# Performance work log

Measured on AMD Instinct MI355X. Metric: run time of the kernel, lower is better.

## Reference

```python
import jax, jax.numpy as jnp
import numpy as np

D_MODEL = 512
D_QK = 512
H = 8
HEAD_DIM = D_QK // H   # 64
V_DIM = D_MODEL // H   # 64
PROJ_OUT = D_MODEL + 2 * D_QK + H  # 1544


def setup_inputs() -> dict:
    key = jax.random.key(0)
    k1, k2, k3, k4, k5 = jax.random.split(key, 5)
    B, S = 2, 2048
    x = jax.random.normal(k1, (B, S, D_MODEL), dtype=jnp.float32)
    s_in = 1.0 / np.sqrt(D_MODEL)
    Wvqkn_w = jax.random.uniform(k2, (PROJ_OUT, D_MODEL), jnp.float32, -s_in, s_in)
    Wvqkn_b = jax.random.uniform(k3, (PROJ_OUT,), jnp.float32, -s_in, s_in)
    out_w = jax.random.uniform(k4, (D_MODEL, D_MODEL), jnp.float32, -s_in, s_in)
    out_b = jax.random.uniform(k5, (D_MODEL,), jnp.float32, -s_in, s_in)
    return {"x": x, "Wvqkn_w": Wvqkn_w, "Wvqkn_b": Wvqkn_b,
            "out_w": out_w, "out_b": out_b}


def reference(x, Wvqkn_w, Wvqkn_b, out_w, out_b):
    B, S, _ = x.shape
    # fused qkvn projection
    vqkn = jnp.einsum('bsd,od->bso', x, Wvqkn_w) + Wvqkn_b  # [B,S,1544]
    v = vqkn[..., :D_MODEL]                                  # [B,S,512]
    qk = vqkn[..., D_MODEL:D_MODEL + 2 * D_QK]               # [B,S,1024]
    n = vqkn[..., D_MODEL + 2 * D_QK:]                       # [B,S,H]
    qk = qk.reshape(B, S, 2, H, HEAD_DIM)
    v = v.reshape(B, S, H, V_DIM)
    q, k = qk[:, :, 0], qk[:, :, 1]                          # approx_fn = identity
    # linear attention via cumulative KV state (scale=1.0, scale_B=False)
    kv = jnp.einsum('bshd,bsht->bshdt', k, v)                # [B,S,H,D,Dv]
    kv = jnp.cumsum(kv, axis=1)
    out = jnp.einsum('bshd,bshdt->bsht', q, kv)              # [B,S,H,Dv]
    # normalization gating: norm_fn = exp, no offset
    gate = jnp.exp(-jnp.exp(n))                              # [B,S,H]
    ctx = gate[..., None] * out
    ctx = ctx.reshape(B, S, D_MODEL)
    return jnp.einsum('bsd,od->bso', ctx, out_w) + out_b
```

## Files before the change

kernel.cpp:

```cpp
#include <hip/hip_runtime.h>
#include <hip/hip_bf16.h>
#include <math.h>

#define B_    2
#define S_    2048
#define DM    512
#define H_    8
#define PROJ  1544
#define NPAD1 1664
#define CHK   64
#define NC    32
#define BS_   4096
#define BH    16

typedef __attribute__((ext_vector_type(8))) short shortx8;
typedef __attribute__((ext_vector_type(4))) short shortx4;
typedef __attribute__((ext_vector_type(4))) float floatx4;

#define GCAST(p) ((const __attribute__((address_space(1))) void*)(p))
#define LCAST(p) ((__attribute__((address_space(3))) void*)(p))

__device__ inline short f2bf(float f) {
    __hip_bfloat16 h = __float2bfloat16(f);
    return *(short*)&h;
}
__device__ inline float bf2f(short s) {
    __hip_bfloat16 h = *(__hip_bfloat16*)&s;
    return __bfloat162float(h);
}
__device__ inline shortx8 read8(const short* buf, int row, int k) {
    return *(const shortx8*)&buf[row * 64 + ((((k >> 3) ^ (row & 7))) << 3)];
}

#define E1 ((size_t)BS_ * DM)
#define E2 ((size_t)NPAD1 * DM)
#define E3 ((size_t)DM * DM)
__global__ __launch_bounds__(256) void convert_all(const float* __restrict__ x,
                                                   const float* __restrict__ w1,
                                                   const float* __restrict__ w2,
                                                   short* __restrict__ xb,
                                                   short* __restrict__ w1b,
                                                   short* __restrict__ w2b) {
    size_t e = ((size_t)blockIdx.x * 256 + threadIdx.x) * 8;
    const float* src;
    short* dst;
    bool zero = false;
    if (e < E1) { src = x + e; dst = xb + e; }
    else if (e < E1 + E2) {
        size_t o = e - E1;
        dst = w1b + o;
        size_t row = o >> 9;
        if (row < PROJ) src = w1 + o; else { src = w1; zero = true; }
    } else if (e < E1 + E2 + E3) {
        size_t o = e - E1 - E2;
        src = w2 + o; dst = w2b + o;
    } else return;
    short out[8];
    if (zero) {
#pragma unroll
        for (int i = 0; i < 8; i++) out[i] = 0;
    } else {
        float4 f0 = *(const float4*)src;
        float4 f1 = *(const float4*)(src + 4);
        out[0] = f2bf(f0.x); out[1] = f2bf(f0.y); out[2] = f2bf(f0.z); out[3] = f2bf(f0.w);
        out[4] = f2bf(f1.x); out[5] = f2bf(f1.y); out[6] = f2bf(f1.z); out[7] = f2bf(f1.w);
    }
    *(shortx8*)dst = *(shortx8*)out;
}

__global__ __launch_bounds__(256) void gemm_mfma64(const short* __restrict__ A,
                                                   const short* __restrict__ Bw,
                                                   const float* __restrict__ bias,
                                                   float* __restrict__ C,
                                                   int N, int K) {
    __shared__ __align__(16) short As[64 * 64];
    __shared__ __align__(16) short Bs[128 * 64];
    const int tid  = threadIdx.x;
    const int wave = tid >> 6, lane = tid & 63;
    const int m0 = blockIdx.y * 64;
    const int n0 = blockIdx.x * 128;
    const int lrow = lane >> 3;
    const int swz  = ((lane & 7) ^ lrow) << 3;
    const int lm = lane & 15, q = lane >> 4;
    const int wc = wave * 32;
    floatx4 acc[4][2] = {};

    const short* gA0 = A  + (size_t)(m0 +      wave * 8 + lrow) * K + swz;
    const short* gA1 = A  + (size_t)(m0 + 32 + wave * 8 + lrow) * K + swz;
    const short* gB[4];
#pragma unroll
    for (int h = 0; h < 4; h++)
        gB[h] = Bw + (size_t)(n0 + h * 32 + wave * 8 + lrow) * K + swz;

    for (int k0 = 0; k0 < K; k0 += 64) {
        __builtin_amdgcn_global_load_lds(GCAST(gA0 + k0), LCAST(&As[(wave * 8) * 64]),        16, 0, 0);
        __builtin_amdgcn_global_load_lds(GCAST(gA1 + k0), LCAST(&As[(32 + wave * 8) * 64]),   16, 0, 0);
#pragma unroll
        for (int h = 0; h < 4; h++)
            __builtin_amdgcn_global_load_lds(GCAST(gB[h] + k0), LCAST(&Bs[(h * 32 + wave * 8) * 64]), 16, 0, 0);
        __syncthreads();
        shortx8 af[2][4], bw[2][2];
#pragma unroll
        for (int ks = 0; ks < 2; ks++) {
#pragma unroll
            for (int i = 0; i < 4; i++) af[ks][i] = read8(As, i * 16 + lm, ks * 32 + q * 8);
#pragma unroll
            for (int j = 0; j < 2; j++) bw[ks][j] = read8(Bs, wc + j * 16 + lm, ks * 32 + q * 8);
        }
#pragma unroll
        for (int ks = 0; ks < 2; ks++)
#pragma unroll
            for (int i = 0; i < 4; i++)
#pragma unroll
                for (int j = 0; j < 2; j++)
                    acc[i][j] = __builtin_amdgcn_mfma_f32_16x16x32_bf16(af[ks][i], bw[ks][j], acc[i][j], 0, 0, 0);
        __syncthreads();
    }
#pragma unroll
    for (int i = 0; i < 4; i++) {
        int rb = m0 + i * 16 + q * 4;
#pragma unroll
        for (int j = 0; j < 2; j++) {
            int col = n0 + wc + j * 16 + lm;
            float bv = bias[col];
#pragma unroll
            for (int r = 0; r < 4; r++)
                C[(size_t)(rb + r) * N + col] = acc[i][j][r] + bv;
        }
    }
}

__global__ __launch_bounds__(256) void gemm1_fused(const short* __restrict__ A,
                                                   const short* __restrict__ Bw,
                                                   const float* __restrict__ bias,
                                                   short* __restrict__ qb,
                                                   short* __restrict__ kb,
                                                   short* __restrict__ kTb,
                                                   short* __restrict__ vTb,
                                                   float* __restrict__ gateb) {
    __shared__ __align__(16) short As[64 * 64];
    __shared__ __align__(16) short Bs[128 * 64];
    const int K = DM;
    const int tid  = threadIdx.x;
    const int wave = tid >> 6, lane = tid & 63;
    const int m0 = blockIdx.y * 64;
    const int n0 = blockIdx.x * 128;
    const int lrow = lane >> 3;
    const int swz  = ((lane & 7) ^ lrow) << 3;
    const int lm = lane & 15, q = lane >> 4;
    const int wc = wave * 32;
    floatx4 acc[4][2] = {};

    const short* gA0 = A  + (size_t)(m0 +      wave * 8 + lrow) * K + swz;
    const short* gA1 = A  + (size_t)(m0 + 32 + wave * 8 + lrow) * K + swz;
    const short* gB[4];
#pragma unroll
    for (int h = 0; h < 4; h++)
        gB[h] = Bw + (size_t)(n0 + h * 32 + wave * 8 + lrow) * K + swz;

    for (int k0 = 0; k0 < K; k0 += 64) {
        __builtin_amdgcn_global_load_lds(GCAST(gA0 + k0), LCAST(&As[(wave * 8) * 64]),        16, 0, 0);
        __builtin_amdgcn_global_load_lds(GCAST(gA1 + k0), LCAST(&As[(32 + wave * 8) * 64]),   16, 0, 0);
#pragma unroll
        for (int h = 0; h < 4; h++)
            __builtin_amdgcn_global_load_lds(GCAST(gB[h] + k0), LCAST(&Bs[(h * 32 + wave * 8) * 64]), 16, 0, 0);
        __syncthreads();
        shortx8 af[2][4], bw[2][2];
#pragma unroll
        for (int ks = 0; ks < 2; ks++) {
#pragma unroll
            for (int i = 0; i < 4; i++) af[ks][i] = read8(As, i * 16 + lm, ks * 32 + q * 8);
#pragma unroll
            for (int j = 0; j < 2; j++) bw[ks][j] = read8(Bs, wc + j * 16 + lm, ks * 32 + q * 8);
        }
#pragma unroll
        for (int ks = 0; ks < 2; ks++)
#pragma unroll
            for (int i = 0; i < 4; i++)
#pragma unroll
                for (int j = 0; j < 2; j++)
                    acc[i][j] = __builtin_amdgcn_mfma_f32_16x16x32_bf16(af[ks][i], bw[ks][j], acc[i][j], 0, 0, 0);
        __syncthreads();
    }

    const int bIdx = m0 >> 11;
    const int bh0  = bIdx * H_;
#pragma unroll
    for (int i = 0; i < 4; i++) {
        int s0 = (m0 & (S_ - 1)) + i * 16 + q * 4;
#pragma unroll
        for (int j = 0; j < 2; j++) {
            int col = n0 + wc + j * 16 + lm;
            float bv = (col < PROJ) ? bias[col] : 0.f;
            float vals[4];
#pragma unroll
            for (int r = 0; r < 4; r++) vals[r] = acc[i][j][r] + bv;
            if (col < 512) {
                int h = col >> 6, vd = col & 63;
                short tmp[4];
#pragma unroll
                for (int r = 0; r < 4; r++) tmp[r] = f2bf(vals[r]);
                *(shortx4*)&vTb[((size_t)(bh0 + h) * 64 + vd) * S_ + s0] = *(shortx4*)tmp;
            } else if (col < 1024) {
                int h = (col >> 6) - 8, d = col & 63;
                size_t rb = ((size_t)(bh0 + h) * S_ + s0) * 64 + d;
#pragma unroll
                for (int r = 0; r < 4; r++) qb[rb + (size_t)r * 64] = f2bf(vals[r]);
            } else if (col < 1536) {
                int h = (col >> 6) - 16, d = col & 63;
                size_t rb = ((size_t)(bh0 + h) * S_ + s0) * 64 + d;
                short tmp[4];
#pragma unroll
                for (int r = 0; r < 4; r++) { tmp[r] = f2bf(vals[r]); kb[rb + (size_t)r * 64] = tmp[r]; }
                *(shortx4*)&kTb[((size_t)(bh0 + h) * 64 + d) * S_ + s0] = *(shortx4*)tmp;
            } else if (col < PROJ) {
                int h = col - 1536;
                float g[4];
#pragma unroll
                for (int r = 0; r < 4; r++) g[r] = __expf(-__expf(vals[r]));
                *(float4*)&gateb[(size_t)(bh0 + h) * S_ + s0] = make_float4(g[0], g[1], g[2], g[3]);
            }
        }
    }
}

__global__ __launch_bounds__(256) void chunk_kv_mfma(const short* __restrict__ vTb,
                                                     const short* __restrict__ kTb,
                                                     float* __restrict__ kvbuf) {
    __shared__ __align__(16) short VT[64 * 64];
    __shared__ __align__(16) short KT[64 * 64];
    const int blk = blockIdx.x;
    const int c = blk & (NC - 1), bh = blk >> 5;
    const int base = c * CHK;
    const int tid = threadIdx.x, wave = tid >> 6, lane = tid & 63;
    const int lrow = lane >> 3, lgrp = lane & 7;

#pragma unroll
    for (int half = 0; half < 2; half++) {
        int v0 = wave * 8 + half * 32;
        int row = v0 + lrow;
        int gcol = ((lgrp ^ (row & 7)) << 3);
        __builtin_amdgcn_global_load_lds(GCAST(vTb + ((size_t)(bh * 64 + row)) * S_ + base + gcol),
                                         LCAST(&VT[v0 * 64]), 16, 0, 0);
        __builtin_amdgcn_global_load_lds(GCAST(kTb + ((size_t)(bh * 64 + row)) * S_ + base + gcol),
                                         LCAST(&KT[v0 * 64]), 16, 0, 0);
    }
    __syncthreads();

    const int lm = lane & 15, q = lane >> 4;
    const int wr = (wave >> 1) * 32, wc = (wave & 1) * 32;
    floatx4 acc[2][2] = {};
#pragma unroll
    for (int ks = 0; ks < 2; ks++) {
        shortx8 a[2], b2[2];
#pragma unroll
        for (int i = 0; i < 2; i++) a[i]  = read8(VT, wr + i * 16 + lm, ks * 32 + q * 8);
#pragma unroll
        for (int j = 0; j < 2; j++) b2[j] = read8(KT, wc + j * 16 + lm, ks * 32 + q * 8);
#pragma unroll
        for (int i = 0; i < 2; i++)
#pragma unroll
            for (int j = 0; j < 2; j++)
                acc[i][j] = __builtin_amdgcn_mfma_f32_16x16x32_bf16(a[i], b2[j], acc[i][j], 0, 0, 0);
    }
    float* outp = kvbuf + ((size_t)blk << 12);
#pragma unroll
    for (int i = 0; i < 2; i++)
#pragma unroll
        for (int j = 0; j < 2; j++)
#pragma unroll
            for (int r = 0; r < 4; r++)
                outp[(wr + i * 16 + q * 4 + r) * 64 + wc + j * 16 + lm] = acc[i][j][r];
}

__global__ __launch_bounds__(256) void scan_groups(const float* __restrict__ kvbuf,
                                                   float* __restrict__ kvg) {
    const int blk = blockIdx.x;
    const int bh = blk >> 4, seg = blk & 15;
    const int e = seg * 256 + threadIdx.x;
    const float* src = kvbuf + (((size_t)bh * NC) << 12) + e;
    float* dst = kvg + (((size_t)bh * 8) << 12) + e;
    float run = 0.f;
#pragma unroll
    for (int g = 0; g < 8; g++) {
        dst[(size_t)g << 12] = run;
#pragma unroll
        for (int cc = 0; cc < 4; cc++)
            run += src[(size_t)(g * 4 + cc) << 12];
    }
}

__global__ __launch_bounds__(256) void attn_mfma(const short* __restrict__ qb,
                                                 const short* __restrict__ kb,
                                                 const short* __restrict__ vTb,
                                                 const float* __restrict__ gateb,
                                                 const float* __restrict__ kvbuf,
                                                 const float* __restrict__ kvg,
                                                 short* __restrict__ ctxb) {
    __shared__ __align__(16) short Qs[64 * 64];
    __shared__ __align__(16) short KsSb[64 * 64];
    __shared__ __align__(16) short VTs[64 * 64];
    __shared__ __align__(16) short Phi[64 * 64];
    __shared__ __align__(16) short Plo[64 * 64];
    const int blk = blockIdx.x;
    const int bh = blk & (BH - 1);
    const int c  = (NC - 1) - (blk >> 4);
    const int base = c * CHK;
    const int tid = threadIdx.x, wave = tid >> 6, lane = tid & 63;
    const int lrow = lane >> 3, lgrp = lane & 7;

#pragma unroll
    for (int half = 0; half < 2; half++) {
        int v0 = wave * 8 + half * 32;
        int row = v0 + lrow;
        int gcol = ((lgrp ^ (row & 7)) << 3);
        __builtin_amdgcn_global_load_lds(GCAST(qb + ((size_t)bh * S_ + base + row) * 64 + gcol),
                                         LCAST(&Qs[v0 * 64]), 16, 0, 0);
        __builtin_amdgcn_global_load_lds(GCAST(kb + ((size_t)bh * S_ + base + row) * 64 + gcol),
                                         LCAST(&KsSb[v0 * 64]), 16, 0, 0);
        __builtin_amdgcn_global_load_lds(GCAST(vTb + ((size_t)(bh * 64 + row)) * S_ + base + gcol),
                                         LCAST(&VTs[v0 * 64]), 16, 0, 0);
    }

    float pacc[16];
    {
        const float* gp = kvg + (((size_t)bh * 8 + (c >> 2)) << 12) + tid;
#pragma unroll
        for (int it = 0; it < 16; it++) pacc[it] = gp[it * 256];
        const float* kvb = kvbuf + (((size_t)bh * NC) << 12) + tid;
        for (int cp = c & ~3; cp < c; cp++) {
            const float* p = kvb + ((size_t)cp << 12);
#pragma unroll
            for (int it = 0; it < 16; it++) pacc[it] += p[it * 256];
        }
    }
#pragma unroll
    for (int it = 0; it < 16; it++) {
        int idx = it * 256 + tid;
        int v = idx >> 6, d = idx & 63;
        float f = pacc[it];
        short hi = f2bf(f);
        short lo = f2bf(f - bf2f(hi));
        int sw = v * 64 + (((d >> 3) ^ (v & 7)) << 3) + (d & 7);
        Phi[sw] = hi; Plo[sw] = lo;
    }
    __syncthreads();

    const int lm = lane & 15, q = lane >> 4;
    const int wr = (wave >> 1) * 32, wc = (wave & 1) * 32;

    floatx4 sacc[2][2] = {};
#pragma unroll
    for (int ks = 0; ks < 2; ks++) {
        shortx8 qa[2], kf[2];
#pragma unroll
        for (int i = 0; i < 2; i++) qa[i] = read8(Qs, wr + i * 16 + lm, ks * 32 + q * 8);
#pragma unroll
        for (int j = 0; j < 2; j++) kf[j] = read8(KsSb, wc + j * 16 + lm, ks * 32 + q * 8);
#pragma unroll
        for (int i = 0; i < 2; i++)
#pragma unroll
            for (int j = 0; j < 2; j++)
                sacc[i][j] = __builtin_amdgcn_mfma_f32_16x16x32_bf16(qa[i], kf[j], sacc[i][j], 0, 0, 0);
    }
    __syncthreads();

#pragma unroll
    for (int i = 0; i < 2; i++)
#pragma unroll
        for (int j = 0; j < 2; j++)
#pragma unroll
            for (int r = 0; r < 4; r++) {
                int s = wr + i * 16 + q * 4 + r;
                int t = wc + j * 16 + lm;
                KsSb[s * 64 + (((t >> 3) ^ (s & 7)) << 3) + (t & 7)] =
                    f2bf(t <= s ? sacc[i][j][r] : 0.f);
            }
    __syncthreads();

    floatx4 oacc[2][2] = {};
#pragma unroll
    for (int ks = 0; ks < 2; ks++) {
        shortx8 sa[2], vb[2];
#pragma unroll
        for (int i = 0; i < 2; i++) sa[i] = read8(KsSb, wr + i * 16 + lm, ks * 32 + q * 8);
#pragma unroll
        for (int j = 0; j < 2; j++) vb[j] = read8(VTs, wc + j * 16 + lm, ks * 32 + q * 8);
#pragma unroll
        for (int i = 0; i < 2; i++)
#pragma unroll
            for (int j = 0; j < 2; j++)
                oacc[i][j] = __builtin_amdgcn_mfma_f32_16x16x32_bf16(sa[i], vb[j], oacc[i][j], 0, 0, 0);
    }
#pragma unroll
    for (int ks = 0; ks < 2; ks++) {
        shortx8 qa[2], ph[2], pl[2];
#pragma unroll
        for (int i = 0; i < 2; i++) qa[i] = read8(Qs, wr + i * 16 + lm, ks * 32 + q * 8);
#pragma unroll
        for (int j = 0; j < 2; j++) {
            ph[j] = read8(Phi, wc + j * 16 + lm, ks * 32 + q * 8);
            pl[j] = read8(Plo, wc + j * 16 + lm, ks * 32 + q * 8);
        }
#pragma unroll
        for (int i = 0; i < 2; i++)
#pragma unroll
            for (int j = 0; j < 2; j++) {
                oacc[i][j] = __builtin_amdgcn_mfma_f32_16x16x32_bf16(qa[i], ph[j], oacc[i][j], 0, 0, 0);
                oacc[i][j] = __builtin_amdgcn_mfma_f32_16x16x32_bf16(qa[i], pl[j], oacc[i][j], 0, 0, 0);
            }
    }
    const size_t tok0 = (size_t)(bh >> 3) * S_ + base;
    const int h = bh & 7;
    const float* gaterow = gateb + (size_t)bh * S_ + base;
#pragma unroll
    for (int i = 0; i < 2; i++)
#pragma unroll
        for (int j = 0; j < 2; j++)
#pragma unroll
            for (int r = 0; r < 4; r++) {
                int s = wr + i * 16 + q * 4 + r;
                int v = wc + j * 16 + lm;
                ctxb[(tok0 + s) * DM + h * 64 + v] = f2bf(gaterow[s] * oacc[i][j][r]);
            }
}

extern "C" void kernel_launch(void* const* d_in, const int* in_sizes, int n_in,
                              void* d_out, int out_size, void* d_ws, size_t ws_size,
                              hipStream_t stream) {
    const float* x       = (const float*)d_in[0];
    const float* Wvqkn_w = (const float*)d_in[1];
    const float* Wvqkn_b = (const float*)d_in[2];
    const float* out_w   = (const float*)d_in[3];
    const float* out_b   = (const float*)d_in[4];
    float* out = (float*)d_out;

    float* kvbuf = (float*)d_ws;
    float* kvg   = kvbuf + (size_t)BH * NC * 4096;
    short* xb    = (short*)(kvg + (size_t)BH * 8 * 4096);
    short* w1b   = xb   + (size_t)BS_ * DM;
    short* w2b   = w1b  + (size_t)NPAD1 * DM;
    short* ctxb  = w2b  + (size_t)DM * DM;
    short* qb    = ctxb + (size_t)BS_ * DM;
    short* kb    = qb   + (size_t)BH * S_ * 64;
    short* kTb   = kb   + (size_t)BH * S_ * 64;
    short* vTb   = kTb  + (size_t)BH * S_ * 64;
    float* gateb = (float*)(vTb + (size_t)BH * S_ * 64);

    convert_all<<<(int)((E1 + E2 + E3) / 8 / 256), 256, 0, stream>>>(
        x, Wvqkn_w, out_w, xb, w1b, w2b);

    gemm1_fused<<<dim3(NPAD1 / 128, BS_ / 64), 256, 0, stream>>>(
        xb, w1b, Wvqkn_b, qb, kb, kTb, vTb, gateb);

    chunk_kv_mfma<<<BH * NC, 256, 0, stream>>>(vTb, kTb, kvbuf);
    scan_groups<<<BH * 16, 256, 0, stream>>>(kvbuf, kvg);
    attn_mfma<<<BH * NC, 256, 0, stream>>>(qb, kb, vTb, gateb, kvbuf, kvg, ctxb);

    gemm_mfma64<<<dim3(DM / 128, BS_ / 64), 256, 0, stream>>>(ctxb, w2b, out_b, out, DM, DM);
}
```

Measured before the change: 110.9 us.

## Fold group scan into chunk KV kernel via in-group running prefix sums

The chunk KV kernel now processes four consecutive chunks per block and keeps the MFMA accumulator across them, so each stored kvbuf entry is an inclusive prefix within its group of four. This lets the separate scan_groups kernel and the kvg buffer be dropped. The attention kernel rebuilds its prefix state by summing the last entry of each earlier group plus the previous chunk's in-group prefix. The cost is fewer blocks in the KV kernel (128 instead of 512), serial work within each block, and up to eight global reads per attention block instead of roughly four.

After: 110.4 us. Within noise of the previous version (-0.5%).

```diff
diff --git a/kernel.cpp b/kernel.cpp
--- a/kernel.cpp
+++ b/kernel.cpp
@@ -224,69 +224,55 @@
     }
 }
 
-__global__ __launch_bounds__(256) void chunk_kv_mfma(const short* __restrict__ vTb,
-                                                     const short* __restrict__ kTb,
-                                                     float* __restrict__ kvbuf) {
+__global__ __launch_bounds__(256) void chunk_kv_grouped(const short* __restrict__ vTb,
+                                                        const short* __restrict__ kTb,
+                                                        float* __restrict__ kvbuf) {
     __shared__ __align__(16) short VT[64 * 64];
     __shared__ __align__(16) short KT[64 * 64];
     const int blk = blockIdx.x;
-    const int c = blk & (NC - 1), bh = blk >> 5;
-    const int base = c * CHK;
+    const int bh = blk >> 3, g = blk & 7;
     const int tid = threadIdx.x, wave = tid >> 6, lane = tid & 63;
     const int lrow = lane >> 3, lgrp = lane & 7;
-
-#pragma unroll
-    for (int half = 0; half < 2; half++) {
-        int v0 = wave * 8 + half * 32;
-        int row = v0 + lrow;
-        int gcol = ((lgrp ^ (row & 7)) << 3);
-        __builtin_amdgcn_global_load_lds(GCAST(vTb + ((size_t)(bh * 64 + row)) * S_ + base + gcol),
-                                         LCAST(&VT[v0 * 64]), 16, 0, 0);
-        __builtin_amdgcn_global_load_lds(GCAST(kTb + ((size_t)(bh * 64 + row)) * S_ + base + gcol),
-                                         LCAST(&KT[v0 * 64]), 16, 0, 0);
-    }
-    __syncthreads();
-
     const int lm = lane & 15, q = lane >> 4;
     const int wr = (wave >> 1) * 32, wc = (wave & 1) * 32;
     floatx4 acc[2][2] = {};
-#pragma unroll
-    for (int ks = 0; ks < 2; ks++) {
-        shortx8 a[2], b2[2];
-#pragma unroll
-        for (int i = 0; i < 2; i++) a[i]  = read8(VT, wr + i * 16 + lm, ks * 32 + q * 8);
-#pragma unroll
-        for (int j = 0; j < 2; j++) b2[j] = read8(KT, wc + j * 16 + lm, ks * 32 + q * 8);
+
+    for (int cc = 0; cc < 4; cc++) {
+        const int c = g * 4 + cc;
+        const int base = c * CHK;
+#pragma unroll
+        for (int half = 0; half < 2; half++) {
+            int v0 = wave * 8 + half * 32;
+            int row = v0 + lrow;
+            int gcol = ((lgrp ^ (row & 7)) << 3);
+            __builtin_amdgcn_global_load_lds(GCAST(vTb + ((size_t)(bh * 64 + row)) * S_ + base + gcol),
+                                             LCAST(&VT[v0 * 64]), 16, 0, 0);
+            __builtin_amdgcn_global_load_lds(GCAST(kTb + ((size_t)(bh * 64 + row)) * S_ + base + gcol),
+                                             LCAST(&KT[v0 * 64]), 16, 0, 0);
+        }
+        __syncthreads();
+#pragma unroll
+        for (int ks = 0; ks < 2; ks++) {
+            shortx8 a[2], b2[2];
+#pragma unroll
+            for (int i = 0; i < 2; i++) a[i]  = read8(VT, wr + i * 16 + lm, ks * 32 + q * 8);
+#pragma unroll
+            for (int j = 0; j < 2; j++) b2[j] = read8(KT, wc + j * 16 + lm, ks * 32 + q * 8);
+#pragma unroll
+            for (int i = 0; i < 2; i++)
+#pragma unroll
+                for (int j = 0; j < 2; j++)
+                    acc[i][j] = __builtin_amdgcn_mfma_f32_16x16x32_bf16(a[i], b2[j], acc[i][j], 0, 0, 0);
+        }
+        float* outp = kvbuf + (((size_t)bh * NC + c) << 12);
 #pragma unroll
         for (int i = 0; i < 2; i++)
 #pragma unroll
             for (int j = 0; j < 2; j++)
-                acc[i][j] = __builtin_amdgcn_mfma_f32_16x16x32_bf16(a[i], b2[j], acc[i][j], 0, 0, 0);
-    }
-    float* outp = kvbuf + ((size_t)blk << 12);
-#pragma unroll
-    for (int i = 0; i < 2; i++)
-#pragma unroll
-        for (int j = 0; j < 2; j++)
-#pragma unroll
-            for (int r = 0; r < 4; r++)
-                outp[(wr + i * 16 + q * 4 + r) * 64 + wc + j * 16 + lm] = acc[i][j][r];
-}
-
-__global__ __launch_bounds__(256) void scan_groups(const float* __restrict__ kvbuf,
-                                                   float* __restrict__ kvg) {
-    const int blk = blockIdx.x;
-    const int bh = blk >> 4, seg = blk & 15;
-    const int e = seg * 256 + threadIdx.x;
-    const float* src = kvbuf + (((size_t)bh * NC) << 12) + e;
-    float* dst = kvg + (((size_t)bh * 8) << 12) + e;
-    float run = 0.f;
-#pragma unroll
-    for (int g = 0; g < 8; g++) {
-        dst[(size_t)g << 12] = run;
-#pragma unroll
-        for (int cc = 0; cc < 4; cc++)
-            run += src[(size_t)(g * 4 + cc) << 12];
+#pragma unroll
+                for (int r = 0; r < 4; r++)
+                    outp[(wr + i * 16 + q * 4 + r) * 64 + wc + j * 16 + lm] = acc[i][j][r];
+        __syncthreads();
     }
 }
 
@@ -295,7 +281,6 @@
                                                  const short* __restrict__ vTb,
                                                  const float* __restrict__ gateb,
                                                  const float* __restrict__ kvbuf,
-                                                 const float* __restrict__ kvg,
                                                  short* __restrict__ ctxb) {
     __shared__ __align__(16) short Qs[64 * 64];
     __shared__ __align__(16) short KsSb[64 * 64];
@@ -322,14 +307,17 @@
                                          LCAST(&VTs[v0 * 64]), 16, 0, 0);
     }
 
-    float pacc[16];
+    float pacc[16] = {};
     {
-        const float* gp = kvg + (((size_t)bh * 8 + (c >> 2)) << 12) + tid;
-#pragma unroll
-        for (int it = 0; it < 16; it++) pacc[it] = gp[it * 256];
         const float* kvb = kvbuf + (((size_t)bh * NC) << 12) + tid;
-        for (int cp = c & ~3; cp < c; cp++) {
-            const float* p = kvb + ((size_t)cp << 12);
+        const int g = c >> 2;
+        for (int gp = 0; gp < g; gp++) {
+            const float* p = kvb + ((size_t)(gp * 4 + 3) << 12);
+#pragma unroll
+            for (int it = 0; it < 16; it++) pacc[it] += p[it * 256];
+        }
+        if (c & 3) {
+            const float* p = kvb + ((size_t)(c - 1) << 12);
 #pragma unroll
             for (int it = 0; it < 16; it++) pacc[it] += p[it * 256];
         }
@@ -436,8 +424,7 @@
     float* out = (float*)d_out;
 
     float* kvbuf = (float*)d_ws;
-    float* kvg   = kvbuf + (size_t)BH * NC * 4096;
-    short* xb    = (short*)(kvg + (size_t)BH * 8 * 4096);
+    short* xb    = (short*)(kvbuf + (size_t)BH * NC * 4096);
     short* w1b   = xb   + (size_t)BS_ * DM;
     short* w2b   = w1b  + (size_t)NPAD1 * DM;
     short* ctxb  = w2b  + (size_t)DM * DM;
@@ -453,9 +440,8 @@
     gemm1_fused<<<dim3(NPAD1 / 128, BS_ / 64), 256, 0, stream>>>(
         xb, w1b, Wvqkn_b, qb, kb, kTb, vTb, gateb);
 
-    chunk_kv_mfma<<<BH * NC, 256, 0, stream>>>(vTb, kTb, kvbuf);
-    scan_groups<<<BH * 16, 256, 0, stream>>>(kvbuf, kvg);
-    attn_mfma<<<BH * NC, 256, 0, stream>>>(qb, kb, vTb, gateb, kvbuf, kvg, ctxb);
+    chunk_kv_grouped<<<BH * 8, 256, 0, stream>>>(vTb, kTb, kvbuf);
+    attn_mfma<<<BH * NC, 256, 0, stream>>>(qb, kb, vTb, gateb, kvbuf, ctxb);
 
     gemm_mfma64<<<dim3(DM / 128, BS_ / 64), 256, 0, stream>>>(ctxb, w2b, out_b, out, DM, DM);
 }
```
